# Kernel optimization log

Measured on AMD Instinct MI355X. Metric: run time of the kernel, lower is better.

Reference implementation:

```python
import jax, jax.numpy as jnp
import numpy as np

N, E, IN_DIM, H, D = 50000, 800000, 64, 8, 8
HD = H * D
CLAMP = 5.0


def setup_inputs() -> dict:
    key = jax.random.key(0)
    ks = jax.random.split(key, 13)
    s_in = 1.0 / np.sqrt(IN_DIM)
    s_hd = 1.0 / np.sqrt(HD)
    return {
        "x": jax.random.normal(ks[0], (N, IN_DIM), jnp.float32),
        "edge_attr": jax.random.normal(ks[1], (E, IN_DIM), jnp.float32),
        "edge_index": jax.random.randint(ks[2], (2, E), 0, N, jnp.int32),
        # torch nn.Linear weights are [out_features, in_features]
        "WQ": jax.random.normal(ks[3], (HD, IN_DIM), jnp.float32) * s_in,
        "WK": jax.random.normal(ks[4], (HD, IN_DIM), jnp.float32) * s_in,
        "WV": jax.random.normal(ks[5], (HD, IN_DIM), jnp.float32) * s_in,
        "WEw": jax.random.normal(ks[6], (HD, IN_DIM), jnp.float32) * s_in,
        "WEb": jax.random.normal(ks[7], (HD, IN_DIM), jnp.float32) * s_in,
        "bEb": jax.random.normal(ks[8], (HD,), jnp.float32) * 0.02,
        "WEo": jax.random.normal(ks[9], (HD, HD), jnp.float32) * s_hd,
        "bEo": jax.random.normal(ks[10], (HD,), jnp.float32) * 0.02,
        "Aw": jax.random.normal(ks[11], (D, H, 1), jnp.float32) * s_hd,
        "BW": jax.random.normal(ks[12], (D, H, D), jnp.float32) * s_hd,
    }


def _scatter_softmax(score, dst, num_nodes):
    # score: [E, H, 1]; softmax over edges grouped by dst node
    mx = jax.ops.segment_max(score, dst, num_segments=num_nodes)  # [N,H,1]
    ex = jnp.exp(score - mx[dst])
    den = jax.ops.segment_sum(ex, dst, num_segments=num_nodes)    # [N,H,1]
    return ex / (den[dst] + 1e-16)


def reference(x, edge_attr, edge_index, WQ, WK, WV, WEw, WEb, bEb, WEo, bEo, Aw, BW):
    n = x.shape[0]
    e = edge_attr.shape[0]
    Qh = (x @ WQ.T).reshape(n, H, D)
    Kh = (x @ WK.T).reshape(n, H, D)
    Vh = (x @ WV.T).reshape(n, H, D)
    Ew = (edge_attr @ WEw.T).reshape(e, H, D)
    Eb = (edge_attr @ WEb.T + bEb).reshape(e, H, D)

    dst, src = edge_index[0], edge_index[1]
    conn1 = (Qh[dst] + Kh[src]) * Ew                       # [E,H,D]
    # sqrt(relu(x)) - sqrt(relu(-x)) == sign(x)*sqrt(|x|)
    conn2 = jnp.sign(conn1) * jnp.sqrt(jnp.abs(conn1))
    conn = conn2 + Eb                                      # act = Identity

    Eo_flat = conn.reshape(e, HD) @ WEo.T + bEo            # Oe output [E, H*D]
    Eo = Eo_flat.reshape(e, H, D)

    score = jnp.einsum('ehd,dhc->ehc', conn, Aw)           # [E,H,1]
    score = jnp.clip(score, -CLAMP, CLAMP)
    score = _scatter_softmax(score, dst, n)

    agg = jax.ops.segment_sum(Vh[src] * score, dst, num_segments=n)   # [N,H,D]
    rowV = jax.ops.segment_sum(Eo * score, dst, num_segments=n)       # [N,H,D]
    rowV = jnp.einsum('nhd,dhc->nhc', rowV, BW)
    h_out = agg + rowV                                     # [N,H,D]
    return (h_out, Eo_flat)
```

## Files before the change

### kernel.cpp

```cpp
#include <hip/hip_runtime.h>

#define NN 50000
#define EE 800000
#define NT8 (EE / 256)
#define NB ((NN + 1023) / 1024)

typedef __attribute__((ext_vector_type(8))) short short8;
typedef __attribute__((ext_vector_type(16))) float f32x16;

static __device__ __forceinline__ unsigned short f2bf(float f) {
    unsigned u = __float_as_uint(f);
    u += 0x7fffu + ((u >> 16) & 1u);
    return (unsigned short)(u >> 16);
}
static __device__ __forceinline__ unsigned cvt_pk(float lo, float hi) {
    unsigned r;
    asm("v_cvt_pk_bf16_f32 %0, %1, %2" : "=v"(r) : "v"(lo), "v"(hi));
    return r;
}
static __device__ __forceinline__ float lo_f(unsigned u) { return __uint_as_float(u << 16); }
static __device__ __forceinline__ float hi_f(unsigned u) { return __uint_as_float(u & 0xffff0000u); }
static __device__ __forceinline__ f32x16 splat16(float v) {
    f32x16 r;
    #pragma unroll
    for (int i = 0; i < 16; ++i) r[i] = v;
    return r;
}

union U8 { short8 v; uint2 u[2]; };

static __device__ __forceinline__ short8 ldsfrag(const unsigned short* rowbase, int k0) {
    U8 t;
    t.u[0] = *(const uint2*)(rowbase + k0);
    t.u[1] = *(const uint2*)(rowbase + k0 + 8);
    return t.v;
}

__global__ __launch_bounds__(256) void qkv_mfma_kernel(
    const float* __restrict__ x,
    const float* __restrict__ WQ, const float* __restrict__ WK, const float* __restrict__ WV,
    float* __restrict__ Qh, float* __restrict__ Kh, float* __restrict__ Vh)
{
    __shared__ unsigned short s_wq[64][68];
    __shared__ unsigned short s_wk[64][68];
    __shared__ unsigned short s_wv[64][68];

    int tid = threadIdx.x;
    #pragma unroll
    for (int t = 0; t < 8; ++t) {
        int idx = (t * 256 + tid) * 2;
        int r = idx >> 6, c = idx & 63;
        float2 w = *(const float2*)(WQ + idx);
        *(unsigned*)&s_wq[r][c] = cvt_pk(w.x, w.y);
        w = *(const float2*)(WK + idx);
        *(unsigned*)&s_wk[r][c] = cvt_pk(w.x, w.y);
        w = *(const float2*)(WV + idx);
        *(unsigned*)&s_wv[r][c] = cvt_pk(w.x, w.y);
    }
    __syncthreads();

    int wid = tid >> 6, lane = tid & 63;
    int m0 = blockIdx.x * 128 + wid * 32;
    int lo5 = lane & 31, hi = lane >> 5;

    int rowi = m0 + lo5;
    const float* arow = x + (size_t)(rowi < NN ? rowi : NN - 1) * 64;
    short8 af[4];
    #pragma unroll
    for (int ks = 0; ks < 4; ++ks) {
        int k0 = ks * 16 + hi * 4;
        float4 a0 = *(const float4*)(arow + k0);
        float4 a1 = *(const float4*)(arow + k0 + 8);
        U8 t;
        t.u[0] = make_uint2(cvt_pk(a0.x, a0.y), cvt_pk(a0.z, a0.w));
        t.u[1] = make_uint2(cvt_pk(a1.x, a1.y), cvt_pk(a1.z, a1.w));
        af[ks] = t.v;
    }

    #pragma unroll
    for (int nt = 0; nt < 2; ++nt) {
        int n = nt * 32 + lo5;
        f32x16 cQ = splat16(0.f), cK = splat16(0.f), cV = splat16(0.f);
        #pragma unroll
        for (int ks = 0; ks < 4; ++ks) {
            int k0 = ks * 16 + hi * 4;
            cQ = __builtin_amdgcn_mfma_f32_32x32x16_bf16(af[ks], ldsfrag(s_wq[n], k0), cQ, 0, 0, 0);
            cK = __builtin_amdgcn_mfma_f32_32x32x16_bf16(af[ks], ldsfrag(s_wk[n], k0), cK, 0, 0, 0);
            cV = __builtin_amdgcn_mfma_f32_32x32x16_bf16(af[ks], ldsfrag(s_wv[n], k0), cV, 0, 0, 0);
        }
        #pragma unroll
        for (int r = 0; r < 16; ++r) {
            int m = (r & 3) + 8 * (r >> 2) + 4 * hi;
            int gm = m0 + m;
            if (gm < NN) {
                Qh[(size_t)gm * 64 + n] = cQ[r];
                Kh[(size_t)gm * 64 + n] = cK[r];
                Vh[(size_t)gm * 64 + n] = cV[r];
            }
        }
    }
}

__global__ __launch_bounds__(256) void hist_kernel(const int* __restrict__ eidx,
                                                   int* __restrict__ cnt)
{
    int e = blockIdx.x * blockDim.x + threadIdx.x;
    atomicAdd(&cnt[eidx[e]], 1);
}

__global__ __launch_bounds__(1024) void scan1_kernel(const int* __restrict__ cnt,
                                                     int* __restrict__ rowstart,
                                                     int* __restrict__ bsum)
{
    __shared__ int buf[1024];
    int tid = threadIdx.x;
    int i = blockIdx.x * 1024 + tid;
    int v = (i < NN) ? cnt[i] : 0;
    buf[tid] = v;
    __syncthreads();
    for (int off = 1; off < 1024; off <<= 1) {
        int t = (tid >= off) ? buf[tid - off] : 0;
        __syncthreads();
        buf[tid] += t;
        __syncthreads();
    }
    if (i < NN) rowstart[i] = buf[tid] - v;
    if (tid == 1023) bsum[blockIdx.x] = buf[1023];
}

__global__ __launch_bounds__(64) void scan2_kernel(const int* __restrict__ bsum,
                                                   int* __restrict__ boff,
                                                   int* __restrict__ rowstart)
{
    int lane = threadIdx.x;
    int v = (lane < NB) ? bsum[lane] : 0;
    int s = v;
    #pragma unroll
    for (int off = 1; off < 64; off <<= 1) {
        int t = __shfl_up(s, off, 64);
        if (lane >= off) s += t;
    }
    if (lane < NB) boff[lane] = s - v;
    if (lane == 63) rowstart[NN] = s;
}

__global__ __launch_bounds__(1024) void scan3_kernel(int* __restrict__ rowstart,
                                                     const int* __restrict__ boff,
                                                     int* __restrict__ cursor)
{
    int i = blockIdx.x * 1024 + threadIdx.x;
    if (i < NN) {
        int r = rowstart[i] + boff[blockIdx.x];
        rowstart[i] = r;
        cursor[i] = r;
    }
}

__global__ __launch_bounds__(256) void scatter_kernel(const int* __restrict__ eidx,
                                                      int* __restrict__ cursor,
                                                      int2* __restrict__ edges_csr,
                                                      int* __restrict__ inv)
{
    int e = blockIdx.x * blockDim.x + threadIdx.x;
    int dst = eidx[e];
    int pos = atomicAdd(&cursor[dst], 1);
    edges_csr[pos] = make_int2(e, eidx[EE + e]);
    inv[e] = pos;
}

__global__ __launch_bounds__(512) void edge_mfma_kernel(
    const float* __restrict__ eattr, const int* __restrict__ eidx,
    const int* __restrict__ inv,
    const float* __restrict__ WEw, const float* __restrict__ WEb, const float* __restrict__ bEb,
    const float* __restrict__ WEo, const float* __restrict__ bEo, const float* __restrict__ Aw,
    const float* __restrict__ Qh, const float* __restrict__ Kh,
    float* __restrict__ Eo_out, float* __restrict__ exbuf)
{
    __shared__ unsigned short s_wew[64][68];
    __shared__ unsigned short s_web[64][68];
    __shared__ unsigned short s_weo[64][68];
    __shared__ unsigned short s_baw[32][68];
    __shared__ unsigned short s_qk[8][32][68];
    __shared__ float s_bEb[64];
    __shared__ float s_bEo[64];

    int tid = threadIdx.x;
    #pragma unroll
    for (int t = 0; t < 4; ++t) {
        int idx = (t * 512 + tid) * 2;
        int r = idx >> 6, c = idx & 63;
        float2 w = *(const float2*)(WEw + idx);
        *(unsigned*)&s_wew[r][c] = cvt_pk(w.x, w.y);
        w = *(const float2*)(WEb + idx);
        *(unsigned*)&s_web[r][c] = cvt_pk(w.x, w.y);
        w = *(const float2*)(WEo + idx);
        *(unsigned*)&s_weo[r][c] = cvt_pk(w.x, w.y);
    }
    #pragma unroll
    for (int t = 0; t < 4; ++t) {
        int idx = t * 512 + tid;
        int n = idx >> 6, k = idx & 63;
        s_baw[n][k] = (n == (k >> 3)) ? f2bf(Aw[(k & 7) * 8 + n]) : (unsigned short)0;
    }
    if (tid < 64) { s_bEb[tid] = bEb[tid]; s_bEo[tid] = bEo[tid]; }
    __syncthreads();

    int wid = tid >> 6, lane = tid & 63;
    int lo5 = lane & 31, hi = lane >> 5;
    int mm = lane >> 4;
    int cc = (lane & 15) * 4;

    for (int tile = blockIdx.x; tile < NT8; tile += gridDim.x) {
        int e0 = tile * 256 + wid * 32;
        int e  = e0 + lo5;
        int pos = inv[e];

        #pragma unroll
        for (int t = 0; t < 8; ++t) {
            int m = t * 4 + mm;
            int em = e0 + m;
            int dst = eidx[em], src = eidx[EE + em];
            float4 q = *(const float4*)(Qh + (size_t)dst * 64 + cc);
            float4 k = *(const float4*)(Kh + (size_t)src * 64 + cc);
            *(uint2*)&s_qk[wid][m][cc] =
                make_uint2(cvt_pk(q.x + k.x, q.y + k.y), cvt_pk(q.z + k.z, q.w + k.w));
        }

        short8 af[4];
        {
            const float* arow = eattr + (size_t)e * 64;
            #pragma unroll
            for (int ks = 0; ks < 4; ++ks) {
                int k0 = ks * 16 + hi * 4;
                float4 a0 = *(const float4*)(arow + k0);
                float4 a1 = *(const float4*)(arow + k0 + 8);
                U8 t;
                t.u[0] = make_uint2(cvt_pk(a0.x, a0.y), cvt_pk(a0.z, a0.w));
                t.u[1] = make_uint2(cvt_pk(a1.x, a1.y), cvt_pk(a1.z, a1.w));
                af[ks] = t.v;
            }
        }

        short8 ca[4];
        #pragma unroll
        for (int nt = 0; nt < 2; ++nt) {
            f32x16 cEw = splat16(0.f), cEb = splat16(0.f);
            #pragma unroll
            for (int ks = 0; ks < 4; ++ks) {
                int k0 = ks * 16 + hi * 4;
                short8 wf = ldsfrag(s_wew[nt * 32 + lo5], k0);
                short8 bf = ldsfrag(s_web[nt * 32 + lo5], k0);
                cEw = __builtin_amdgcn_mfma_f32_32x32x16_bf16(wf, af[ks], cEw, 0, 0, 0);
                cEb = __builtin_amdgcn_mfma_f32_32x32x16_bf16(bf, af[ks], cEb, 0, 0, 0);
            }
            float conn[16];
            #pragma unroll
            for (int r4 = 0; r4 < 4; ++r4) {
                int off = nt * 32 + r4 * 8 + hi * 4;
                uint2 qraw = *(const uint2*)&s_qk[wid][lo5][off];
                float4 bb = *(const float4*)&s_bEb[off];
                float qk[4] = {lo_f(qraw.x), hi_f(qraw.x), lo_f(qraw.y), hi_f(qraw.y)};
                float bbv[4] = {bb.x, bb.y, bb.z, bb.w};
                #pragma unroll
                for (int c = 0; c < 4; ++c) {
                    int r = r4 * 4 + c;
                    float c1 = qk[c] * cEw[r];
                    float c2 = copysignf(sqrtf(fabsf(c1)), c1);
                    conn[r] = c2 + cEb[r] + bbv[c];
                }
            }
            U8 t0, t1;
            t0.u[0] = make_uint2(cvt_pk(conn[0], conn[1]), cvt_pk(conn[2], conn[3]));
            t0.u[1] = make_uint2(cvt_pk(conn[4], conn[5]), cvt_pk(conn[6], conn[7]));
            t1.u[0] = make_uint2(cvt_pk(conn[8], conn[9]), cvt_pk(conn[10], conn[11]));
            t1.u[1] = make_uint2(cvt_pk(conn[12], conn[13]), cvt_pk(conn[14], conn[15]));
            ca[2 * nt + 0] = t0.v;
            ca[2 * nt + 1] = t1.v;
        }

        {
            f32x16 cS = splat16(0.f);
            #pragma unroll
            for (int ks = 0; ks < 4; ++ks) {
                int k0 = ks * 16 + hi * 4;
                cS = __builtin_amdgcn_mfma_f32_32x32x16_bf16(ldsfrag(s_baw[lo5], k0), ca[ks], cS, 0, 0, 0);
            }
            float4 exv;
            exv.x = __expf(fminf(fmaxf(cS[0], -5.0f), 5.0f));
            exv.y = __expf(fminf(fmaxf(cS[1], -5.0f), 5.0f));
            exv.z = __expf(fminf(fmaxf(cS[2], -5.0f), 5.0f));
            exv.w = __expf(fminf(fmaxf(cS[3], -5.0f), 5.0f));
            *(float4*)(exbuf + (size_t)pos * 8 + hi * 4) = exv;
        }

        #pragma unroll
        for (int nt = 0; nt < 2; ++nt) {
            f32x16 cO = splat16(0.f);
            #pragma unroll
            for (int ks = 0; ks < 4; ++ks) {
                int k0 = ks * 16 + hi * 4;
                cO = __builtin_amdgcn_mfma_f32_32x32x16_bf16(ldsfrag(s_weo[nt * 32 + lo5], k0), ca[ks], cO, 0, 0, 0);
            }
            #pragma unroll
            for (int r4 = 0; r4 < 4; ++r4) {
                int off = nt * 32 + r4 * 8 + hi * 4;
                float4 bo = *(const float4*)&s_bEo[off];
                float4 o = make_float4(cO[r4 * 4 + 0] + bo.x, cO[r4 * 4 + 1] + bo.y,
                                       cO[r4 * 4 + 2] + bo.z, cO[r4 * 4 + 3] + bo.w);
                *(float4*)(Eo_out + (size_t)e * 64 + off) = o;
            }
        }
    }
}

__global__ __launch_bounds__(256) void node_kernel(
    const int* __restrict__ rowstart, const int2* __restrict__ edges_csr,
    const float* __restrict__ exbuf, const float* __restrict__ Eo,
    const float* __restrict__ Vh, const float* __restrict__ BW,
    float* __restrict__ hout)
{
    int n = (blockIdx.x * blockDim.x + threadIdx.x) >> 6;
    int lane = threadIdx.x & 63;
    int h = lane >> 3, d = lane & 7;

    int beg = rowstart[n], end = rowstart[n + 1];
    float agg0 = 0.f, rv0 = 0.f, den0 = 0.f;
    float agg1 = 0.f, rv1 = 0.f, den1 = 0.f;
    int j = beg;
    for (; j + 1 < end; j += 2) {
        int2 ea = edges_csr[j];
        int2 eb = edges_csr[j + 1];
        float xa = exbuf[(size_t)j * 8 + h];
        float xb = exbuf[(size_t)(j + 1) * 8 + h];
        agg0 = fmaf(xa, Vh[(size_t)ea.y * 64 + lane], agg0);
        rv0  = fmaf(xa, Eo[(size_t)ea.x * 64 + lane], rv0);
        den0 += xa;
        agg1 = fmaf(xb, Vh[(size_t)eb.y * 64 + lane], agg1);
        rv1  = fmaf(xb, Eo[(size_t)eb.x * 64 + lane], rv1);
        den1 += xb;
    }
    if (j < end) {
        int2 ea = edges_csr[j];
        float xa = exbuf[(size_t)j * 8 + h];
        agg0 = fmaf(xa, Vh[(size_t)ea.y * 64 + lane], agg0);
        rv0  = fmaf(xa, Eo[(size_t)ea.x * 64 + lane], rv0);
        den0 += xa;
    }
    float agg = agg0 + agg1, rv = rv0 + rv1, den = den0 + den1;
    float inv = (den > 0.f) ? (1.0f / den) : 0.f;

    float acc = agg;
    #pragma unroll
    for (int dd = 0; dd < 8; ++dd) {
        float rvd = __shfl(rv, (h << 3) + dd, 64);
        acc = fmaf(rvd, BW[dd * 64 + (h << 3) + d], acc);
    }
    hout[(size_t)n * 64 + lane] = acc * inv;
}

extern "C" void kernel_launch(void* const* d_in, const int* in_sizes, int n_in,
                              void* d_out, int out_size, void* d_ws, size_t ws_size,
                              hipStream_t stream)
{
    const float* x    = (const float*)d_in[0];
    const float* ea   = (const float*)d_in[1];
    const int*   eidx = (const int*)  d_in[2];
    const float* WQ   = (const float*)d_in[3];
    const float* WK   = (const float*)d_in[4];
    const float* WV   = (const float*)d_in[5];
    const float* WEw  = (const float*)d_in[6];
    const float* WEb  = (const float*)d_in[7];
    const float* bEb  = (const float*)d_in[8];
    const float* WEo  = (const float*)d_in[9];
    const float* bEo  = (const float*)d_in[10];
    const float* Aw   = (const float*)d_in[11];
    const float* BW   = (const float*)d_in[12];

    float* hout   = (float*)d_out;
    float* Eo_out = hout + (size_t)NN * 64;

    float* Qh    = (float*)d_ws;
    float* Kh    = Qh + (size_t)NN * 64;
    float* Vh    = Kh + (size_t)NN * 64;
    float* exbuf = Vh + (size_t)NN * 64;
    int* cnt      = (int*)(exbuf + (size_t)EE * 8);
    int* rowstart = cnt + NN;
    int2* edges_csr = (int2*)(rowstart + NN + 2);
    int* invp     = (int*)(edges_csr + EE);
    int* bsum     = invp + EE;
    int* boff     = bsum + 64;

    hipMemsetAsync(cnt, 0, (size_t)NN * sizeof(int), stream);

    hist_kernel<<<EE / 256, 256, 0, stream>>>(eidx, cnt);
    scan1_kernel<<<NB, 1024, 0, stream>>>(cnt, rowstart, bsum);
    scan2_kernel<<<1, 64, 0, stream>>>(bsum, boff, rowstart);
    scan3_kernel<<<NB, 1024, 0, stream>>>(rowstart, boff, cnt);
    scatter_kernel<<<EE / 256, 256, 0, stream>>>(eidx, cnt, edges_csr, invp);

    qkv_mfma_kernel<<<(NN + 127) / 128, 256, 0, stream>>>(x, WQ, WK, WV, Qh, Kh, Vh);

    edge_mfma_kernel<<<512, 512, 0, stream>>>(ea, eidx, invp, WEw, WEb, bEb,
                                              WEo, bEo, Aw, Qh, Kh, Eo_out, exbuf);

    node_kernel<<<(NN * 64) / 256, 256, 0, stream>>>(rowstart, edges_csr,
                                                     exbuf, Eo_out, Vh, BW, hout);
}
```

Measured before the change: 367.9 us.

## Gather Q+K directly into registers and use nontemporal loads/stores for edge streams

Drops the cooperative LDS staging of Q[dst]+K[src] rows. Each lane now loads its own edge's Q and K values straight into registers in fp32, which also removes the bf16 rounding of the sum. Edge attribute loads, Eo stores and the Eo gathers in the node kernel become nontemporal to limit cache pollution from streaming data. The trade-offs are higher register pressure from the 32-float qks array and less coalesced per-lane gathers.

```diff
diff --git a/kernel.cpp b/kernel.cpp
--- a/kernel.cpp
+++ b/kernel.cpp
@@ -7,6 +7,7 @@
 
 typedef __attribute__((ext_vector_type(8))) short short8;
 typedef __attribute__((ext_vector_type(16))) float f32x16;
+typedef __attribute__((ext_vector_type(4))) float f32x4;
 
 static __device__ __forceinline__ unsigned short f2bf(float f) {
     unsigned u = __float_as_uint(f);
@@ -18,8 +19,6 @@
     asm("v_cvt_pk_bf16_f32 %0, %1, %2" : "=v"(r) : "v"(lo), "v"(hi));
     return r;
 }
-static __device__ __forceinline__ float lo_f(unsigned u) { return __uint_as_float(u << 16); }
-static __device__ __forceinline__ float hi_f(unsigned u) { return __uint_as_float(u & 0xffff0000u); }
 static __device__ __forceinline__ f32x16 splat16(float v) {
     f32x16 r;
     #pragma unroll
@@ -180,7 +179,6 @@
     __shared__ unsigned short s_web[64][68];
     __shared__ unsigned short s_weo[64][68];
     __shared__ unsigned short s_baw[32][68];
-    __shared__ unsigned short s_qk[8][32][68];
     __shared__ float s_bEb[64];
     __shared__ float s_bEo[64];
 
@@ -207,37 +205,40 @@
 
     int wid = tid >> 6, lane = tid & 63;
     int lo5 = lane & 31, hi = lane >> 5;
-    int mm = lane >> 4;
-    int cc = (lane & 15) * 4;
 
     for (int tile = blockIdx.x; tile < NT8; tile += gridDim.x) {
         int e0 = tile * 256 + wid * 32;
         int e  = e0 + lo5;
         int pos = inv[e];
-
-        #pragma unroll
-        for (int t = 0; t < 8; ++t) {
-            int m = t * 4 + mm;
-            int em = e0 + m;
-            int dst = eidx[em], src = eidx[EE + em];
-            float4 q = *(const float4*)(Qh + (size_t)dst * 64 + cc);
-            float4 k = *(const float4*)(Kh + (size_t)src * 64 + cc);
-            *(uint2*)&s_qk[wid][m][cc] =
-                make_uint2(cvt_pk(q.x + k.x, q.y + k.y), cvt_pk(q.z + k.z, q.w + k.w));
-        }
+        int dst = eidx[e], src = eidx[EE + e];
 
         short8 af[4];
         {
-            const float* arow = eattr + (size_t)e * 64;
+            const f32x4* arow = (const f32x4*)(eattr + (size_t)e * 64);
             #pragma unroll
             for (int ks = 0; ks < 4; ++ks) {
-                int k0 = ks * 16 + hi * 4;
-                float4 a0 = *(const float4*)(arow + k0);
-                float4 a1 = *(const float4*)(arow + k0 + 8);
+                int q4 = (ks * 16 + hi * 4) >> 2;
+                f32x4 a0 = __builtin_nontemporal_load(arow + q4);
+                f32x4 a1 = __builtin_nontemporal_load(arow + q4 + 2);
                 U8 t;
                 t.u[0] = make_uint2(cvt_pk(a0.x, a0.y), cvt_pk(a0.z, a0.w));
                 t.u[1] = make_uint2(cvt_pk(a1.x, a1.y), cvt_pk(a1.z, a1.w));
                 af[ks] = t.v;
+            }
+        }
+        float qks[32];
+        {
+            const float* qrow = Qh + (size_t)dst * 64;
+            const float* krow = Kh + (size_t)src * 64;
+            #pragma unroll
+            for (int q8 = 0; q8 < 8; ++q8) {
+                int off = q8 * 8 + hi * 4;
+                float4 qv = *(const float4*)(qrow + off);
+                float4 kv = *(const float4*)(krow + off);
+                qks[q8 * 4 + 0] = qv.x + kv.x;
+                qks[q8 * 4 + 1] = qv.y + kv.y;
+                qks[q8 * 4 + 2] = qv.z + kv.z;
+                qks[q8 * 4 + 3] = qv.w + kv.w;
             }
         }
 
@@ -257,14 +258,12 @@
             #pragma unroll
             for (int r4 = 0; r4 < 4; ++r4) {
                 int off = nt * 32 + r4 * 8 + hi * 4;
-                uint2 qraw = *(const uint2*)&s_qk[wid][lo5][off];
                 float4 bb = *(const float4*)&s_bEb[off];
-                float qk[4] = {lo_f(qraw.x), hi_f(qraw.x), lo_f(qraw.y), hi_f(qraw.y)};
                 float bbv[4] = {bb.x, bb.y, bb.z, bb.w};
                 #pragma unroll
                 for (int c = 0; c < 4; ++c) {
                     int r = r4 * 4 + c;
-                    float c1 = qk[c] * cEw[r];
+                    float c1 = qks[nt * 16 + r] * cEw[r];
                     float c2 = copysignf(sqrtf(fabsf(c1)), c1);
                     conn[r] = c2 + cEb[r] + bbv[c];
                 }
@@ -305,9 +304,12 @@
             for (int r4 = 0; r4 < 4; ++r4) {
                 int off = nt * 32 + r4 * 8 + hi * 4;
                 float4 bo = *(const float4*)&s_bEo[off];
-                float4 o = make_float4(cO[r4 * 4 + 0] + bo.x, cO[r4 * 4 + 1] + bo.y,
-                                       cO[r4 * 4 + 2] + bo.z, cO[r4 * 4 + 3] + bo.w);
-                *(float4*)(Eo_out + (size_t)e * 64 + off) = o;
+                f32x4 o;
+                o.x = cO[r4 * 4 + 0] + bo.x;
+                o.y = cO[r4 * 4 + 1] + bo.y;
+                o.z = cO[r4 * 4 + 2] + bo.z;
+                o.w = cO[r4 * 4 + 3] + bo.w;
+                __builtin_nontemporal_store(o, (f32x4*)(Eo_out + (size_t)e * 64 + off));
             }
         }
     }
@@ -333,17 +335,17 @@
         float xa = exbuf[(size_t)j * 8 + h];
         float xb = exbuf[(size_t)(j + 1) * 8 + h];
         agg0 = fmaf(xa, Vh[(size_t)ea.y * 64 + lane], agg0);
-        rv0  = fmaf(xa, Eo[(size_t)ea.x * 64 + lane], rv0);
+        rv0  = fmaf(xa, __builtin_nontemporal_load(Eo + (size_t)ea.x * 64 + lane), rv0);
         den0 += xa;
         agg1 = fmaf(xb, Vh[(size_t)eb.y * 64 + lane], agg1);
-        rv1  = fmaf(xb, Eo[(size_t)eb.x * 64 + lane], rv1);
+        rv1  = fmaf(xb, __builtin_nontemporal_load(Eo + (size_t)eb.x * 64 + lane), rv1);
         den1 += xb;
     }
     if (j < end) {
         int2 ea = edges_csr[j];
         float xa = exbuf[(size_t)j * 8 + h];
         agg0 = fmaf(xa, Vh[(size_t)ea.y * 64 + lane], agg0);
-        rv0  = fmaf(xa, Eo[(size_t)ea.x * 64 + lane], rv0);
+        rv0  = fmaf(xa, __builtin_nontemporal_load(Eo + (size_t)ea.x * 64 + lane), rv0);
         den0 += xa;
     }
     float agg = agg0 + agg1, rv = rv0 + rv1, den = den0 + den1;
```

Result: slower. 490.7 us (+33.4%).
